# Optimization experiments

Measured on AMD Instinct MI355X. Metric: run time of the kernel, lower is better.

The kernel has to match this reference:

```python
import jax, jax.numpy as jnp
import numpy as np

DIM = 1024
HEADS = 16
HEAD_DIM = DIM // HEADS
HIDDEN = 4 * DIM
EPS = 1e-5


def layer_norm(x, g, b):
    mu = jnp.mean(x, axis=-1, keepdims=True)
    var = jnp.var(x, axis=-1, keepdims=True)
    return (x - mu) * jax.lax.rsqrt(var + EPS) * g + b


def setup_inputs() -> dict:
    key = jax.random.key(0)
    ks = jax.random.split(key, 8)
    B, N, C = 2, 2048, DIM
    # xavier-uniform-ish scales
    s_qkv = float(np.sqrt(6.0 / (C + 3 * C)))
    s_proj = float(np.sqrt(6.0 / (C + C)))
    s_fc1 = float(np.sqrt(6.0 / (C + HIDDEN)))
    return {
        "x": jax.random.normal(ks[0], (B, N, C), jnp.float32),
        "w_qkv": jax.random.uniform(ks[1], (3 * C, C), jnp.float32, -s_qkv, s_qkv),
        "w_proj": jax.random.uniform(ks[2], (C, C), jnp.float32, -s_proj, s_proj),
        "b_proj": jnp.zeros((C,), jnp.float32),
        "ln1_g": jnp.ones((C,), jnp.float32),
        "ln1_b": jnp.zeros((C,), jnp.float32),
        "ln2_g": jnp.ones((C,), jnp.float32),
        "ln2_b": jnp.zeros((C,), jnp.float32),
        "w_fc1": jax.random.uniform(ks[3], (HIDDEN, C), jnp.float32, -s_fc1, s_fc1),
        "b_fc1": jnp.zeros((HIDDEN,), jnp.float32),
        "w_fc2": jax.random.uniform(ks[4], (C, HIDDEN), jnp.float32, -s_fc1, s_fc1),
        "b_fc2": jnp.zeros((C,), jnp.float32),
    }


def attention(x, w_qkv, w_proj, b_proj):
    B, N, C = x.shape
    qkv = x @ w_qkv.T  # [B,N,3C]
    qkv = qkv.reshape(B, N, 3, HEADS, HEAD_DIM).transpose(2, 0, 3, 1, 4)
    q, k, v = qkv[0], qkv[1], qkv[2]  # [B,H,N,hd]
    scale = HEAD_DIM ** -0.5
    attn = jnp.einsum("bhqd,bhkd->bhqk", q, k) * scale
    attn = jax.nn.softmax(attn, axis=-1)
    out = jnp.einsum("bhqk,bhkd->bhqd", attn, v)  # [B,H,N,hd]
    out = out.transpose(0, 2, 1, 3).reshape(B, N, C)
    return out @ w_proj.T + b_proj


def reference(x, w_qkv, w_proj, b_proj, ln1_g, ln1_b, ln2_g, ln2_b, w_fc1, b_fc1, w_fc2, b_fc2):
    x = x + attention(layer_norm(x, ln1_g, ln1_b), w_qkv, w_proj, b_proj)
    h = layer_norm(x, ln2_g, ln2_b)
    h = jax.nn.gelu(h @ w_fc1.T + b_fc1, approximate=False)
    x = x + (h @ w_fc2.T + b_fc2)
    return x
```

## Files before the change

### kernel.cpp

```cpp
#include <hip/hip_runtime.h>
#include <hip/hip_bf16.h>
#include <math.h>

typedef __bf16 bf16;
typedef __attribute__((ext_vector_type(8))) __bf16 bf16x8;
typedef __attribute__((ext_vector_type(4))) __bf16 bf16x4;
typedef __attribute__((ext_vector_type(4))) float f32x4;

#define DEV static __device__ __forceinline__

typedef const void __attribute__((address_space(1)))* gptr_t;
typedef void __attribute__((address_space(3)))* lptr_t;

DEV void async16(const void* g, void* l) {
  __builtin_amdgcn_global_load_lds((gptr_t)g, (lptr_t)l, 16, 0, 0);
}

DEV void wg_barrier() {
  __builtin_amdgcn_sched_barrier(0);
  __builtin_amdgcn_s_barrier();
  __builtin_amdgcn_sched_barrier(0);
}

__global__ __launch_bounds__(256) void f2b4_kernel(const float* __restrict__ s0,
                                                   const float* __restrict__ s1,
                                                   const float* __restrict__ s2,
                                                   const float* __restrict__ s3,
                                                   bf16* __restrict__ d0, bf16* __restrict__ d1,
                                                   bf16* __restrict__ d2, bf16* __restrict__ d3,
                                                   int n0, int n1, int n2, int n3) {
  int i = (blockIdx.x * 256 + threadIdx.x) * 4;
  const float* s;
  bf16* d;
  int off;
  if (i < n0) { s = s0; d = d0; off = i; }
  else if (i < n0 + n1) { s = s1; d = d1; off = i - n0; }
  else if (i < n0 + n1 + n2) { s = s2; d = d2; off = i - n0 - n1; }
  else if (i < n0 + n1 + n2 + n3) { s = s3; d = d3; off = i - n0 - n1 - n2; }
  else return;
  float4 v = *(const float4*)(s + off);
  d[off + 0] = (bf16)v.x;
  d[off + 1] = (bf16)v.y;
  d[off + 2] = (bf16)v.z;
  d[off + 3] = (bf16)v.w;
}

__global__ __launch_bounds__(256) void ln_kernel(const float* __restrict__ in,
                                                 const float* __restrict__ g,
                                                 const float* __restrict__ b,
                                                 bf16* __restrict__ out) {
  const int row = blockIdx.x;
  const int tid = threadIdx.x;
  float4 v = ((const float4*)(in + (size_t)row * 1024))[tid];
  float s = v.x + v.y + v.z + v.w;
  float s2 = v.x * v.x + v.y * v.y + v.z * v.z + v.w * v.w;
#pragma unroll
  for (int off = 1; off < 64; off <<= 1) {
    s += __shfl_xor(s, off);
    s2 += __shfl_xor(s2, off);
  }
  __shared__ float red[8];
  int w = tid >> 6, lane = tid & 63;
  if (lane == 0) { red[w] = s; red[4 + w] = s2; }
  __syncthreads();
  s = red[0] + red[1] + red[2] + red[3];
  s2 = red[4] + red[5] + red[6] + red[7];
  const float mean = s * (1.f / 1024.f);
  const float var = s2 * (1.f / 1024.f) - mean * mean;
  const float rstd = rsqrtf(var + 1e-5f);
  float4 gv = ((const float4*)g)[tid];
  float4 bv = ((const float4*)b)[tid];
  bf16* orow = out + (size_t)row * 1024 + tid * 4;
  orow[0] = (bf16)((v.x - mean) * rstd * gv.x + bv.x);
  orow[1] = (bf16)((v.y - mean) * rstd * gv.y + bv.y);
  orow[2] = (bf16)((v.z - mean) * rstd * gv.z + bv.z);
  orow[3] = (bf16)((v.w - mean) * rstd * gv.w + bv.w);
}

template <int EPI>
__global__ __launch_bounds__(512, 2) void gemm256(const bf16* __restrict__ A,
                                                  const bf16* __restrict__ B,
                                                  bf16* __restrict__ outb,
                                                  const float* __restrict__ bias,
                                                  int M, int N, int K, int gridN) {
  __shared__ bf16 As[2][256 * 64];
  __shared__ bf16 Bs[2][256 * 64];
  const int nwg = gridDim.x;
  const int bid = blockIdx.x;
  const int swz = (bid & 7) * (nwg >> 3) + (bid >> 3);
  const int bx = swz % gridN, by = swz / gridN;
  const int brow = by * 256, bcol = bx * 256;
  const int tid = threadIdx.x;
  const int lane = tid & 63, wid = tid >> 6;
  const int wm = wid >> 2, wn = wid & 3;
  const int lr = lane & 15, lk4 = lane >> 4;
  const int strow = tid >> 3, stc = tid & 7;
  const int NT = K >> 6;
  f32x4 acc[8][4] = {};

#define STAGE(tt, bb)                                                                   \
  {                                                                                     \
    const int k0_ = (tt)*64;                                                            \
    _Pragma("unroll") for (int s_ = 0; s_ < 4; ++s_) {                                  \
      const int r_ = s_ * 64 + strow;                                                   \
      const int g_ = (stc ^ (strow & 7)) * 8;                                           \
      async16(A + (size_t)(brow + r_) * K + k0_ + g_, &As[bb][r_ * 64 + stc * 8]);      \
      async16(B + (size_t)(bcol + r_) * K + k0_ + g_, &Bs[bb][r_ * 64 + stc * 8]);      \
    }                                                                                   \
  }

  STAGE(0, 0);
  STAGE(1, 1);
  asm volatile("s_waitcnt vmcnt(8)" ::: "memory");
  wg_barrier();

  for (int t = 0; t < NT; ++t) {
    const int cur = t & 1;
    bf16x8 af[8][2], bfr[4][2];
#pragma unroll
    for (int m = 0; m < 8; ++m)
#pragma unroll
      for (int kk = 0; kk < 2; ++kk) {
        const int row = wm * 128 + m * 16 + lr;
        const int kc = kk * 4 + lk4;
        af[m][kk] = *(const bf16x8*)&As[cur][row * 64 + ((kc ^ (row & 7)) * 8)];
      }
#pragma unroll
    for (int n = 0; n < 4; ++n)
#pragma unroll
      for (int kk = 0; kk < 2; ++kk) {
        const int row = wn * 64 + n * 16 + lr;
        const int kc = kk * 4 + lk4;
        bfr[n][kk] = *(const bf16x8*)&Bs[cur][row * 64 + ((kc ^ (row & 7)) * 8)];
      }
    asm volatile("s_waitcnt lgkmcnt(0)" ::: "memory");
    wg_barrier();
    if (t + 2 < NT) STAGE(t + 2, cur);
    __builtin_amdgcn_s_setprio(1);
#pragma unroll
    for (int m = 0; m < 8; ++m)
#pragma unroll
      for (int n = 0; n < 4; ++n) {
        acc[m][n] = __builtin_amdgcn_mfma_f32_16x16x32_bf16(af[m][0], bfr[n][0], acc[m][n], 0, 0, 0);
        acc[m][n] = __builtin_amdgcn_mfma_f32_16x16x32_bf16(af[m][1], bfr[n][1], acc[m][n], 0, 0, 0);
      }
    __builtin_amdgcn_s_setprio(0);
    if (t + 1 < NT) {
      if (t + 2 < NT) {
        asm volatile("s_waitcnt vmcnt(8)" ::: "memory");
      } else {
        asm volatile("s_waitcnt vmcnt(0)" ::: "memory");
      }
      wg_barrier();
    }
  }
#undef STAGE
  const int r0 = brow + wm * 128 + lk4 * 4;
  const int c0 = bcol + wn * 64 + lr;
  float bias_v[4];
  if (EPI == 1) {
#pragma unroll
    for (int n = 0; n < 4; ++n) bias_v[n] = bias[c0 + n * 16];
  }
#pragma unroll
  for (int m = 0; m < 8; ++m)
#pragma unroll
    for (int n = 0; n < 4; ++n)
#pragma unroll
      for (int j = 0; j < 4; ++j) {
        const int r = r0 + m * 16 + j;
        const int c = c0 + n * 16;
        float v = acc[m][n][j];
        if (EPI == 1) {
          v += bias_v[n];
          v = 0.5f * v * (1.0f + erff(v * 0.70710678118654752f));
        }
        outb[(size_t)r * N + c] = (bf16)v;
      }
}

__global__ __launch_bounds__(512, 2) void gemm128(const bf16* __restrict__ A,
                                                  const bf16* __restrict__ B,
                                                  float* __restrict__ outf,
                                                  const float* __restrict__ bias,
                                                  const float* __restrict__ resid,
                                                  int M, int N, int K, int gridN) {
  __shared__ bf16 As[2][128 * 64];
  __shared__ bf16 Bs[2][128 * 64];
  const int nwg = gridDim.x;
  const int bid = blockIdx.x;
  const int swz = (bid & 7) * (nwg >> 3) + (bid >> 3);
  const int bx = swz % gridN, by = swz / gridN;
  const int brow = by * 128, bcol = bx * 128;
  const int tid = threadIdx.x;
  const int lane = tid & 63, wid = tid >> 6;
  const int wm = wid >> 2, wn = wid & 3;
  const int lr = lane & 15, lk4 = lane >> 4;
  const int strow = tid >> 3, stc = tid & 7;
  const int NT = K >> 6;
  f32x4 acc[4][2] = {};

#define STAGE1(tt, bb)                                                                  \
  {                                                                                     \
    const int k0_ = (tt)*64;                                                            \
    _Pragma("unroll") for (int s_ = 0; s_ < 2; ++s_) {                                  \
      const int r_ = s_ * 64 + strow;                                                   \
      const int g_ = (stc ^ (strow & 7)) * 8;                                           \
      async16(A + (size_t)(brow + r_) * K + k0_ + g_, &As[bb][r_ * 64 + stc * 8]);      \
      async16(B + (size_t)(bcol + r_) * K + k0_ + g_, &Bs[bb][r_ * 64 + stc * 8]);      \
    }                                                                                   \
  }

  STAGE1(0, 0);
  STAGE1(1, 1);
  asm volatile("s_waitcnt vmcnt(4)" ::: "memory");
  wg_barrier();

  for (int t = 0; t < NT; ++t) {
    const int cur = t & 1;
    bf16x8 af[4][2], bfr[2][2];
#pragma unroll
    for (int m = 0; m < 4; ++m)
#pragma unroll
      for (int kk = 0; kk < 2; ++kk) {
        const int row = wm * 64 + m * 16 + lr;
        const int kc = kk * 4 + lk4;
        af[m][kk] = *(const bf16x8*)&As[cur][row * 64 + ((kc ^ (row & 7)) * 8)];
      }
#pragma unroll
    for (int n = 0; n < 2; ++n)
#pragma unroll
      for (int kk = 0; kk < 2; ++kk) {
        const int row = wn * 32 + n * 16 + lr;
        const int kc = kk * 4 + lk4;
        bfr[n][kk] = *(const bf16x8*)&Bs[cur][row * 64 + ((kc ^ (row & 7)) * 8)];
      }
    asm volatile("s_waitcnt lgkmcnt(0)" ::: "memory");
    wg_barrier();
    if (t + 2 < NT) STAGE1(t + 2, cur);
    __builtin_amdgcn_s_setprio(1);
#pragma unroll
    for (int m = 0; m < 4; ++m)
#pragma unroll
      for (int n = 0; n < 2; ++n) {
        acc[m][n] = __builtin_amdgcn_mfma_f32_16x16x32_bf16(af[m][0], bfr[n][0], acc[m][n], 0, 0, 0);
        acc[m][n] = __builtin_amdgcn_mfma_f32_16x16x32_bf16(af[m][1], bfr[n][1], acc[m][n], 0, 0, 0);
      }
    __builtin_amdgcn_s_setprio(0);
    if (t + 1 < NT) {
      if (t + 2 < NT) {
        asm volatile("s_waitcnt vmcnt(4)" ::: "memory");
      } else {
        asm volatile("s_waitcnt vmcnt(0)" ::: "memory");
      }
      wg_barrier();
    }
  }
#undef STAGE1
  const int r0 = brow + wm * 64 + lk4 * 4;
  const int c0 = bcol + wn * 32 + lr;
#pragma unroll
  for (int m = 0; m < 4; ++m)
#pragma unroll
    for (int n = 0; n < 2; ++n)
#pragma unroll
      for (int j = 0; j < 4; ++j) {
        const int r = r0 + m * 16 + j;
        const int c = c0 + n * 16;
        outf[(size_t)r * N + c] = acc[m][n][j] + bias[c] + resid[(size_t)r * N + c];
      }
}

__global__ __launch_bounds__(256, 4) void flash_kernel(const bf16* __restrict__ qkv,
                                                       bf16* __restrict__ out) {
  const int qt = blockIdx.x;
  const int bh = blockIdx.y;
  const int b = bh >> 4, h = bh & 15;
  const int tid = threadIdx.x;
  const int lane = tid & 63, w = tid >> 6;
  const int lr = lane & 15, lk4 = lane >> 4;
  const bf16* Qp = qkv + (size_t)(b * 2048) * 3072 + h * 64;
  const bf16* Kp = Qp + 1024;
  const bf16* Vp = Qp + 2048;
  __shared__ bf16 Ks[2][64 * 64];
  __shared__ bf16 VTs[2][64 * 64];
  __shared__ bf16 Ps[64 * 64];
  const int qw0 = qt * 64 + w * 16;
  const float SC = 0.125f * 1.44269504f;
  const float THRU = 8.0f / SC;
  bf16x8 qf[2];
#pragma unroll
  for (int kk = 0; kk < 2; ++kk)
    qf[kk] = *(const bf16x8*)(Qp + (size_t)(qw0 + lr) * 3072 + kk * 32 + lk4 * 8);
  f32x4 o[4] = {};
  float mrun = -1e30f, lrun = 0.f;
  const int sr = tid >> 3, sc8 = tid & 7;
  const int vd = tid & 63, vkc = (tid >> 6) * 16, vc0 = vkc >> 3;
  const int prow = (w * 16 + lr) * 64;
  bf16 vv[16];
#pragma unroll
  for (int i = 0; i < 2; ++i) {
    const int r = i * 32 + sr;
    async16(Kp + (size_t)r * 3072 + (sc8 ^ (r & 7)) * 8, &Ks[0][r * 64 + sc8 * 8]);
  }
#pragma unroll
  for (int j = 0; j < 16; ++j) vv[j] = Vp[(size_t)(vkc + j) * 3072 + vd];
  {
    bf16x8 a, c;
#pragma unroll
    for (int j = 0; j < 8; ++j) { a[j] = vv[j]; c[j] = vv[8 + j]; }
    *(bf16x8*)&VTs[0][vd * 64 + ((vc0 ^ (vd & 7)) * 8)] = a;
    *(bf16x8*)&VTs[0][vd * 64 + (((vc0 + 1) ^ (vd & 7)) * 8)] = c;
  }
  __syncthreads();
  for (int t = 0; t < 32; ++t) {
    const int cur = t & 1, nxt = cur ^ 1;
    if (t < 31) {
      const size_t kv0n = (size_t)(t + 1) * 64;
#pragma unroll
      for (int i = 0; i < 2; ++i) {
        const int r = i * 32 + sr;
        async16(Kp + (kv0n + r) * 3072 + (sc8 ^ (r & 7)) * 8, &Ks[nxt][r * 64 + sc8 * 8]);
      }
#pragma unroll
      for (int j = 0; j < 16; ++j) vv[j] = Vp[(kv0n + vkc + j) * 3072 + vd];
    }
    f32x4 st[4] = {};
    __builtin_amdgcn_s_setprio(1);
#pragma unroll
    for (int n = 0; n < 4; ++n)
#pragma unroll
      for (int kk = 0; kk < 2; ++kk) {
        bf16x8 kf = *(const bf16x8*)&Ks[cur][(n * 16 + lr) * 64 + (((kk * 4 + lk4) ^ (lr & 7)) * 8)];
        st[n] = __builtin_amdgcn_mfma_f32_16x16x32_bf16(kf, qf[kk], st[n], 0, 0, 0);
      }
    __builtin_amdgcn_s_setprio(0);
    float mx = -1e30f;
#pragma unroll
    for (int n = 0; n < 4; ++n)
#pragma unroll
      for (int j = 0; j < 4; ++j) mx = fmaxf(mx, st[n][j]);
    mx = fmaxf(mx, __shfl_xor(mx, 16));
    mx = fmaxf(mx, __shfl_xor(mx, 32));
    const bool skip = __all(mx <= mrun + THRU);
    const float mn = skip ? mrun : fmaxf(mrun, mx);
    const float mnS = mn * SC;
    float rs = 0.f;
#pragma unroll
    for (int n = 0; n < 4; ++n) {
      float p0 = exp2f(fmaf(st[n][0], SC, -mnS));
      float p1 = exp2f(fmaf(st[n][1], SC, -mnS));
      float p2 = exp2f(fmaf(st[n][2], SC, -mnS));
      float p3 = exp2f(fmaf(st[n][3], SC, -mnS));
      rs += (p0 + p1) + (p2 + p3);
      bf16x4 pk;
      pk[0] = (bf16)p0; pk[1] = (bf16)p1; pk[2] = (bf16)p2; pk[3] = (bf16)p3;
      *(bf16x4*)&Ps[prow + (((n * 2 + (lk4 >> 1)) ^ (lr & 7)) * 8) + (lk4 & 1) * 4] = pk;
    }
    rs += __shfl_xor(rs, 16);
    rs += __shfl_xor(rs, 32);
    if (!skip) {
      const float alpha = exp2f(fmaf(mrun, SC, -mnS));
      lrun = lrun * alpha + rs;
      mrun = mn;
#pragma unroll
      for (int c = 0; c < 4; ++c)
#pragma unroll
        for (int j = 0; j < 4; ++j) o[c][j] *= alpha;
    } else {
      lrun += rs;
    }
    bf16x8 pb[2];
#pragma unroll
    for (int kk = 0; kk < 2; ++kk)
      pb[kk] = *(const bf16x8*)&Ps[prow + (((kk * 4 + lk4) ^ (lr & 7)) * 8)];
    __builtin_amdgcn_s_setprio(1);
#pragma unroll
    for (int c = 0; c < 4; ++c)
#pragma unroll
      for (int kk = 0; kk < 2; ++kk) {
        bf16x8 vfr = *(const bf16x8*)&VTs[cur][(c * 16 + lr) * 64 + (((kk * 4 + lk4) ^ (lr & 7)) * 8)];
        o[c] = __builtin_amdgcn_mfma_f32_16x16x32_bf16(vfr, pb[kk], o[c], 0, 0, 0);
      }
    __builtin_amdgcn_s_setprio(0);
    if (t < 31) {
      bf16x8 a, c;
#pragma unroll
      for (int j = 0; j < 8; ++j) { a[j] = vv[j]; c[j] = vv[8 + j]; }
      *(bf16x8*)&VTs[nxt][vd * 64 + ((vc0 ^ (vd & 7)) * 8)] = a;
      *(bf16x8*)&VTs[nxt][vd * 64 + (((vc0 + 1) ^ (vd & 7)) * 8)] = c;
    }
    __syncthreads();
  }
  const float inv = 1.f / lrun;
#pragma unroll
  for (int c = 0; c < 4; ++c) {
    bf16x4 ov;
#pragma unroll
    for (int j = 0; j < 4; ++j) ov[j] = (bf16)(o[c][j] * inv);
    *(bf16x4*)&out[(size_t)(b * 2048 + qw0 + lr) * 1024 + h * 64 + c * 16 + lk4 * 4] = ov;
  }
}

extern "C" void kernel_launch(void* const* d_in, const int* in_sizes, int n_in,
                              void* d_out, int out_size, void* d_ws, size_t ws_size,
                              hipStream_t stream) {
  const float* x      = (const float*)d_in[0];
  const float* w_qkv  = (const float*)d_in[1];
  const float* w_proj = (const float*)d_in[2];
  const float* b_proj = (const float*)d_in[3];
  const float* ln1_g  = (const float*)d_in[4];
  const float* ln1_b  = (const float*)d_in[5];
  const float* ln2_g  = (const float*)d_in[6];
  const float* ln2_b  = (const float*)d_in[7];
  const float* w_fc1  = (const float*)d_in[8];
  const float* b_fc1  = (const float*)d_in[9];
  const float* w_fc2  = (const float*)d_in[10];
  const float* b_fc2  = (const float*)d_in[11];

  char* W = (char*)d_ws;
  bf16* wqkvb = (bf16*)(W + 0);
  bf16* wprojb = (bf16*)(W + 6291456);
  bf16* wfc1b = (bf16*)(W + 8388608);
  bf16* wfc2b = (bf16*)(W + 16777216);
  bf16* xn    = (bf16*)(W + 25165824);
  bf16* qkvb  = (bf16*)(W + 33554432);
  bf16* attnb = (bf16*)(W + 58720256);
  float* x2   = (float*)(W + 67108864);
  bf16* hbuf  = (bf16*)(W + 83886080);
  float* outf = (float*)d_out;

  f2b4_kernel<<<12288, 256, 0, stream>>>(w_qkv, w_proj, w_fc1, w_fc2,
                                         wqkvb, wprojb, wfc1b, wfc2b,
                                         3145728, 1048576, 4194304, 4194304);

  ln_kernel<<<4096, 256, 0, stream>>>(x, ln1_g, ln1_b, xn);
  gemm256<0><<<192, 512, 0, stream>>>(xn, wqkvb, qkvb, nullptr, 4096, 3072, 1024, 12);
  flash_kernel<<<dim3(32, 32), 256, 0, stream>>>(qkvb, attnb);
  gemm128<<<256, 512, 0, stream>>>(attnb, wprojb, x2, b_proj, x, 4096, 1024, 1024, 8);
  ln_kernel<<<4096, 256, 0, stream>>>(x2, ln2_g, ln2_b, xn);
  gemm256<1><<<256, 512, 0, stream>>>(xn, wfc1b, hbuf, b_fc1, 4096, 4096, 1024, 16);
  gemm128<<<256, 512, 0, stream>>>(hbuf, wfc2b, outf, b_fc2, x2, 4096, 1024, 4096, 8);
}
```

Measured before the change: 255.2 us.

## Double flash-attention query tile to 128 rows with 512-thread blocks sharing K/V

The flash attention kernel now processes 128 query rows per block using 8 waves instead of 64 rows with 4 waves, halving the grid. Each K/V tile loaded into LDS is reused by twice as many waves, and the per-thread K/V load work is halved, which cuts global K/V traffic and load instructions per query row. The row-max reduction is also rewritten as a tree. The trade-off is fewer blocks (512) and larger LDS per block, which may lower occupancy or wave-level parallelism.

```diff
diff --git a/kernel.cpp b/kernel.cpp
--- a/kernel.cpp
+++ b/kernel.cpp
@@ -271,7 +271,7 @@
       }
 }
 
-__global__ __launch_bounds__(256, 4) void flash_kernel(const bf16* __restrict__ qkv,
+__global__ __launch_bounds__(512, 4) void flash_kernel(const bf16* __restrict__ qkv,
                                                        bf16* __restrict__ out) {
   const int qt = blockIdx.x;
   const int bh = blockIdx.y;
@@ -284,8 +284,8 @@
   const bf16* Vp = Qp + 2048;
   __shared__ bf16 Ks[2][64 * 64];
   __shared__ bf16 VTs[2][64 * 64];
-  __shared__ bf16 Ps[64 * 64];
-  const int qw0 = qt * 64 + w * 16;
+  __shared__ bf16 Ps[128 * 64];
+  const int qw0 = qt * 128 + w * 16;
   const float SC = 0.125f * 1.44269504f;
   const float THRU = 8.0f / SC;
   bf16x8 qf[2];
@@ -295,35 +295,27 @@
   f32x4 o[4] = {};
   float mrun = -1e30f, lrun = 0.f;
   const int sr = tid >> 3, sc8 = tid & 7;
-  const int vd = tid & 63, vkc = (tid >> 6) * 16, vc0 = vkc >> 3;
+  const int vd = tid & 63, vkc = (tid >> 6) * 8;
+  const int vch = tid >> 6;
   const int prow = (w * 16 + lr) * 64;
-  bf16 vv[16];
-#pragma unroll
-  for (int i = 0; i < 2; ++i) {
-    const int r = i * 32 + sr;
-    async16(Kp + (size_t)r * 3072 + (sc8 ^ (r & 7)) * 8, &Ks[0][r * 64 + sc8 * 8]);
-  }
-#pragma unroll
-  for (int j = 0; j < 16; ++j) vv[j] = Vp[(size_t)(vkc + j) * 3072 + vd];
+  bf16 vv[8];
+  async16(Kp + (size_t)sr * 3072 + (sc8 ^ (sr & 7)) * 8, &Ks[0][sr * 64 + sc8 * 8]);
+#pragma unroll
+  for (int j = 0; j < 8; ++j) vv[j] = Vp[(size_t)(vkc + j) * 3072 + vd];
   {
-    bf16x8 a, c;
-#pragma unroll
-    for (int j = 0; j < 8; ++j) { a[j] = vv[j]; c[j] = vv[8 + j]; }
-    *(bf16x8*)&VTs[0][vd * 64 + ((vc0 ^ (vd & 7)) * 8)] = a;
-    *(bf16x8*)&VTs[0][vd * 64 + (((vc0 + 1) ^ (vd & 7)) * 8)] = c;
+    bf16x8 a;
+#pragma unroll
+    for (int j = 0; j < 8; ++j) a[j] = vv[j];
+    *(bf16x8*)&VTs[0][vd * 64 + ((vch ^ (vd & 7)) * 8)] = a;
   }
   __syncthreads();
   for (int t = 0; t < 32; ++t) {
     const int cur = t & 1, nxt = cur ^ 1;
     if (t < 31) {
       const size_t kv0n = (size_t)(t + 1) * 64;
-#pragma unroll
-      for (int i = 0; i < 2; ++i) {
-        const int r = i * 32 + sr;
-        async16(Kp + (kv0n + r) * 3072 + (sc8 ^ (r & 7)) * 8, &Ks[nxt][r * 64 + sc8 * 8]);
-      }
-#pragma unroll
-      for (int j = 0; j < 16; ++j) vv[j] = Vp[(kv0n + vkc + j) * 3072 + vd];
+      async16(Kp + (kv0n + sr) * 3072 + (sc8 ^ (sr & 7)) * 8, &Ks[nxt][sr * 64 + sc8 * 8]);
+#pragma unroll
+      for (int j = 0; j < 8; ++j) vv[j] = Vp[(kv0n + vkc + j) * 3072 + vd];
     }
     f32x4 st[4] = {};
     __builtin_amdgcn_s_setprio(1);
@@ -335,11 +327,11 @@
         st[n] = __builtin_amdgcn_mfma_f32_16x16x32_bf16(kf, qf[kk], st[n], 0, 0, 0);
       }
     __builtin_amdgcn_s_setprio(0);
-    float mx = -1e30f;
-#pragma unroll
-    for (int n = 0; n < 4; ++n)
-#pragma unroll
-      for (int j = 0; j < 4; ++j) mx = fmaxf(mx, st[n][j]);
+    float m01 = fmaxf(fmaxf(st[0][0], st[0][1]), fmaxf(st[0][2], st[0][3]));
+    float m23 = fmaxf(fmaxf(st[1][0], st[1][1]), fmaxf(st[1][2], st[1][3]));
+    float m45 = fmaxf(fmaxf(st[2][0], st[2][1]), fmaxf(st[2][2], st[2][3]));
+    float m67 = fmaxf(fmaxf(st[3][0], st[3][1]), fmaxf(st[3][2], st[3][3]));
+    float mx = fmaxf(fmaxf(m01, m23), fmaxf(m45, m67));
     mx = fmaxf(mx, __shfl_xor(mx, 16));
     mx = fmaxf(mx, __shfl_xor(mx, 32));
     const bool skip = __all(mx <= mrun + THRU);
@@ -384,11 +376,10 @@
       }
     __builtin_amdgcn_s_setprio(0);
     if (t < 31) {
-      bf16x8 a, c;
-#pragma unroll
-      for (int j = 0; j < 8; ++j) { a[j] = vv[j]; c[j] = vv[8 + j]; }
-      *(bf16x8*)&VTs[nxt][vd * 64 + ((vc0 ^ (vd & 7)) * 8)] = a;
-      *(bf16x8*)&VTs[nxt][vd * 64 + (((vc0 + 1) ^ (vd & 7)) * 8)] = c;
+      bf16x8 a;
+#pragma unroll
+      for (int j = 0; j < 8; ++j) a[j] = vv[j];
+      *(bf16x8*)&VTs[nxt][vd * 64 + ((vch ^ (vd & 7)) * 8)] = a;
     }
     __syncthreads();
   }
@@ -436,7 +427,7 @@
 
   ln_kernel<<<4096, 256, 0, stream>>>(x, ln1_g, ln1_b, xn);
   gemm256<0><<<192, 512, 0, stream>>>(xn, wqkvb, qkvb, nullptr, 4096, 3072, 1024, 12);
-  flash_kernel<<<dim3(32, 32), 256, 0, stream>>>(qkvb, attnb);
+  flash_kernel<<<dim3(16, 32), 512, 0, stream>>>(qkvb, attnb);
   gemm128<<<256, 512, 0, stream>>>(attnb, wprojb, x2, b_proj, x, 4096, 1024, 1024, 8);
   ln_kernel<<<4096, 256, 0, stream>>>(x2, ln2_g, ln2_b, xn);
   gemm256<1><<<256, 512, 0, stream>>>(xn, wfc1b, hbuf, b_fc1, 4096, 4096, 1024, 16);
```

Result: no change. 253.2 us (-0.8%).
